# Kernel optimization log

Measured on AMD Instinct MI355X. Metric: run time of the kernel, lower is better.

## Reference

```python
import jax, jax.numpy as jnp
import numpy as np

ALPHA = 0.25   # FOCAL_LOSS_ALPHA
GAMMA = 2.0    # FOCAL_LOSS_GAMMA


def pairwise_iou(anchor, boxes):
    # anchor [A,4], boxes [M,4] -> [A,M]
    area_b = (boxes[:, 2] - boxes[:, 0]) * (boxes[:, 3] - boxes[:, 1])        # [M]
    area_a = (anchor[:, 2] - anchor[:, 0]) * (anchor[:, 3] - anchor[:, 1])    # [A]
    iw = jnp.clip(jnp.minimum(anchor[:, None, 2], boxes[None, :, 2]) -
                  jnp.maximum(anchor[:, None, 0], boxes[None, :, 0]), 0.0)
    ih = jnp.clip(jnp.minimum(anchor[:, None, 3], boxes[None, :, 3]) -
                  jnp.maximum(anchor[:, None, 1], boxes[None, :, 1]), 0.0)
    inter = iw * ih
    ua = jnp.clip(area_a[:, None] + area_b[None, :] - inter, 1e-8)
    return inter / ua


def _per_image(cls_pred, reg_pred, ann, anchor, aw, ah, acx, acy):
    # cls_pred [A,C], reg_pred [A,4], ann [M,5]
    valid = ann[:, 4] != -1.0                              # padding mask
    p = jnp.clip(cls_pred, 1e-4, 1.0 - 1e-4)
    iou = pairwise_iou(anchor, ann[:, :4])                 # [A,M]
    iou = jnp.where(valid[None, :], iou, -1.0)             # invalid GT never matched
    iou_max = iou.max(axis=1)
    iou_arg = iou.argmax(axis=1)
    assigned = ann[iou_arg]                                # [A,5]
    pos = iou_max >= 0.5
    num_pos = pos.sum().astype(p.dtype)
    C = p.shape[1]
    one_hot = jax.nn.one_hot(assigned[:, 4].astype(jnp.int32), C, dtype=p.dtype)
    # targets: 1 for assigned class on positives, 0 elsewhere on positives,
    # 0 everywhere for IoU<0.4, -1 (ignore) in between
    targets = jnp.where(pos[:, None], one_hot,
                        jnp.where((iou_max < 0.4)[:, None], 0.0, -1.0))
    af = jnp.where(targets == 1.0, ALPHA, 1.0 - ALPHA)
    fw = jnp.where(targets == 1.0, 1.0 - p, p)
    fw = af * fw ** GAMMA
    bce = -(targets * jnp.log(p) + (1.0 - targets) * jnp.log(1.0 - p))
    cls_loss = jnp.where(targets != -1.0, fw * bce, 0.0).sum() / jnp.maximum(num_pos, 1.0)
    gw = assigned[:, 2] - assigned[:, 0]
    gh = assigned[:, 3] - assigned[:, 1]
    gcx = assigned[:, 0] + 0.5 * gw
    gcy = assigned[:, 1] + 0.5 * gh
    gw = jnp.maximum(gw, 1.0)
    gh = jnp.maximum(gh, 1.0)
    t = jnp.stack([(gcx - acx) / aw, (gcy - acy) / ah,
                   jnp.log(gw / aw), jnp.log(gh / ah)], axis=1)
    t = t / jnp.array([[0.1, 0.1, 0.2, 0.2]], dtype=p.dtype)
    diff = jnp.abs(t - reg_pred)
    rl = jnp.where(diff <= 1.0 / 9.0, 0.5 * 9.0 * diff ** 2, diff - 0.5 / 9.0)
    reg_loss = jnp.where(num_pos > 0,
                         (rl * pos[:, None]).sum() / jnp.maximum(4.0 * num_pos, 1.0),
                         0.0)
    return cls_loss, reg_loss


def setup_inputs() -> dict:
    key = jax.random.key(0)
    kc, kr, ka1, ka2, kb1, kb2, kl = jax.random.split(key, 7)
    B, A, C, M = 8, 120000, 80, 32
    classifications = jax.random.uniform(kc, (B, A, C), jnp.float32, 0.001, 0.999)
    regressions = jax.random.normal(kr, (B, A, 4), jnp.float32)
    # anchors: valid boxes with x1<x2, y1<y2
    xy1 = jax.random.uniform(ka1, (1, A, 2), jnp.float32, 0.0, 700.0)
    wh = jax.random.uniform(ka2, (1, A, 2), jnp.float32, 8.0, 200.0)
    anchors = jnp.concatenate([xy1, xy1 + wh], axis=-1)
    # annotations: [B,M,5], last 8 slots per image padded with -1
    gxy1 = jax.random.uniform(kb1, (B, M, 2), jnp.float32, 0.0, 600.0)
    gwh = jax.random.uniform(kb2, (B, M, 2), jnp.float32, 16.0, 250.0)
    labels = jax.random.randint(kl, (B, M, 1), 0, C).astype(jnp.float32)
    annotations = jnp.concatenate([gxy1, gxy1 + gwh, labels], axis=-1)
    pad = jnp.arange(M) >= (M - 8)
    annotations = jnp.where(pad[None, :, None], -1.0, annotations)
    return {"classifications": classifications, "regressions": regressions,
            "anchors": anchors, "annotations": annotations}


def reference(classifications, regressions, anchors, annotations):
    anchor = anchors[0]
    aw = anchor[:, 2] - anchor[:, 0]
    ah = anchor[:, 3] - anchor[:, 1]
    acx = anchor[:, 0] + 0.5 * aw
    acy = anchor[:, 1] + 0.5 * ah
    cls_l, reg_l = jax.vmap(_per_image, in_axes=(0, 0, 0, None, None, None, None, None))(
        classifications, regressions, annotations, anchor, aw, ah, acx, acy)
    return cls_l.mean(keepdims=True), reg_l.mean(keepdims=True)
```

## Files before the change

### kernel.cpp

```cpp
#include <hip/hip_runtime.h>
#include <hip/hip_bf16.h>

constexpr int B_   = 8;
constexpr int A_   = 120000;
constexpr int C_   = 80;
constexpr int M_   = 32;
constexpr int APB  = 256;
constexpr int C4   = C_ / 4;
constexpr int GX   = (A_ + APB - 1) / APB;

#define F_LN2 0.69314718056f
#define C0_ (0.75f * F_LN2)
#define C1_ (0.25f * F_LN2)

typedef float vfloat4 __attribute__((ext_vector_type(4)));


__device__ __forceinline__ float smooth_l1(float d) {
    return (d <= (1.0f / 9.0f)) ? 4.5f * d * d : d - (0.5f / 9.0f);
}

__device__ __forceinline__ float clampp(float x) {
    return fminf(fmaxf(x, 1e-4f), 1.0f - 1e-4f);
}

__device__ __forceinline__ float f_neg(float p) {
    return C0_ * p * p * (-__log2f(1.0f - p));
}
__device__ __forceinline__ float f_pos(float p) {
    const float q = 1.0f - p;
    return C1_ * q * q * (-__log2f(p));
}

__global__ __launch_bounds__(256) void focal_fused(
    const float* __restrict__ cls,
    const float* __restrict__ reg,
    const float* __restrict__ anc,
    const float* __restrict__ ann,
    float* __restrict__ P_cls,
    float* __restrict__ P_reg,
    float* __restrict__ P_np)
{
    __shared__ float s_ann[M_ * 5];
    __shared__ float s_mask[APB];
    __shared__ float s_red[3][4];

    const int b   = blockIdx.y;
    const int a0  = blockIdx.x * APB;
    const int tid = threadIdx.x;
    const int na  = min(APB, A_ - a0);

    if (tid < M_ * 5) s_ann[tid] = ann[b * M_ * 5 + tid];
    __syncthreads();

    float acc  = 0.0f;
    float rsum = 0.0f;
    float npos = 0.0f;

    if (tid < na) {
        const int a = a0 + tid;
        const float4 ab = reinterpret_cast<const float4*>(anc)[a];
        const float ax1 = ab.x, ay1 = ab.y, ax2 = ab.z, ay2 = ab.w;
        const float area_a = (ax2 - ax1) * (ay2 - ay1);

        float best = -2.0f;
        int   arg  = 0;
        #pragma unroll 8
        for (int m = 0; m < M_; ++m) {
            const float bx1 = s_ann[m * 5 + 0];
            const float by1 = s_ann[m * 5 + 1];
            const float bx2 = s_ann[m * 5 + 2];
            const float by2 = s_ann[m * 5 + 3];
            const float lab = s_ann[m * 5 + 4];
            float iw = fmaxf(fminf(ax2, bx2) - fmaxf(ax1, bx1), 0.0f);
            float ih = fmaxf(fminf(ay2, by2) - fmaxf(ay1, by1), 0.0f);
            const float inter  = iw * ih;
            const float area_b = (bx2 - bx1) * (by2 - by1);
            const float ua = fmaxf(area_a + area_b - inter, 1e-8f);
            float iou = inter / ua;
            if (lab == -1.0f) iou = -1.0f;
            if (iou > best) { best = iou; arg = m; }
        }

        float mask = 1.0f;
        if (best >= 0.5f) {
            const int code = (int)s_ann[arg * 5 + 4];
            const float gx1 = s_ann[arg * 5 + 0];
            const float gy1 = s_ann[arg * 5 + 1];
            const float gx2 = s_ann[arg * 5 + 2];
            const float gy2 = s_ann[arg * 5 + 3];
            float gw = gx2 - gx1, gh = gy2 - gy1;
            const float gcx = gx1 + 0.5f * gw;
            const float gcy = gy1 + 0.5f * gh;
            gw = fmaxf(gw, 1.0f);
            gh = fmaxf(gh, 1.0f);
            const float aw  = ax2 - ax1, ah = ay2 - ay1;
            const float acx = ax1 + 0.5f * aw;
            const float acy = ay1 + 0.5f * ah;
            const float t0 = ((gcx - acx) / aw) * 10.0f;
            const float t1 = ((gcy - acy) / ah) * 10.0f;
            const float t2 = logf(gw / aw) * 5.0f;
            const float t3 = logf(gh / ah) * 5.0f;
            const float4 rp = reinterpret_cast<const float4*>(reg)[(size_t)b * A_ + a];
            rsum = smooth_l1(fabsf(t0 - rp.x))
                 + smooth_l1(fabsf(t1 - rp.y))
                 + smooth_l1(fabsf(t2 - rp.z))
                 + smooth_l1(fabsf(t3 - rp.w));
            npos = 1.0f;
            const float p = clampp(cls[((size_t)b * A_ + a) * C_ + code]);
            acc = f_pos(p) - f_neg(p);
        } else if (best >= 0.4f) {
            mask = 0.0f;
        }
        s_mask[tid] = mask;
    }
    __syncthreads();

    const vfloat4* cp = reinterpret_cast<const vfloat4*>(cls) + ((size_t)b * A_ + a0) * C4;
    const int total = na * C4;
    #pragma unroll 4
    for (int t = tid; t < total; t += APB) {
        const int la = t / C4;
        const float m = s_mask[la];
        const vfloat4 v = __builtin_nontemporal_load(&cp[t]);
        float s = f_neg(clampp(v.x));
        s += f_neg(clampp(v.y));
        s += f_neg(clampp(v.z));
        s += f_neg(clampp(v.w));
        acc = fmaf(m, s, acc);
    }

    #pragma unroll
    for (int off = 32; off > 0; off >>= 1) {
        acc  += __shfl_down(acc,  off, 64);
        rsum += __shfl_down(rsum, off, 64);
        npos += __shfl_down(npos, off, 64);
    }
    const int wv = tid >> 6;
    if ((tid & 63) == 0) {
        s_red[0][wv] = acc;
        s_red[1][wv] = rsum;
        s_red[2][wv] = npos;
    }
    __syncthreads();
    if (tid == 0) {
        const int slot = b * GX + blockIdx.x;
        P_cls[slot] = s_red[0][0] + s_red[0][1] + s_red[0][2] + s_red[0][3];
        P_reg[slot] = s_red[1][0] + s_red[1][1] + s_red[1][2] + s_red[1][3];
        P_np [slot] = s_red[2][0] + s_red[2][1] + s_red[2][2] + s_red[2][3];
    }
}

__global__ __launch_bounds__(1024) void focal_finalize(
    const float* __restrict__ P_cls,
    const float* __restrict__ P_reg,
    const float* __restrict__ P_np,
    float* __restrict__ out)
{
    __shared__ float red[3][16];
    const int tid  = threadIdx.x;
    const int lane = tid & 63;
    const int wv   = tid >> 6;
    float cm = 0.0f, rm = 0.0f;

    for (int b = 0; b < B_; ++b) {
        float c = 0.0f, r = 0.0f, n = 0.0f;
        for (int x = tid; x < GX; x += 1024) {
            c += P_cls[b * GX + x];
            r += P_reg[b * GX + x];
            n += P_np [b * GX + x];
        }
        #pragma unroll
        for (int off = 32; off > 0; off >>= 1) {
            c += __shfl_down(c, off, 64);
            r += __shfl_down(r, off, 64);
            n += __shfl_down(n, off, 64);
        }
        if (lane == 0) { red[0][wv] = c; red[1][wv] = r; red[2][wv] = n; }
        __syncthreads();
        if (tid == 0) {
            float cs = 0.0f, rs = 0.0f, ns = 0.0f;
            #pragma unroll
            for (int w = 0; w < 16; ++w) { cs += red[0][w]; rs += red[1][w]; ns += red[2][w]; }
            cm += cs / fmaxf(ns, 1.0f);
            rm += (ns > 0.0f) ? rs / fmaxf(4.0f * ns, 1.0f) : 0.0f;
        }
        __syncthreads();
    }
    if (tid == 0) {
        out[0] = cm / (float)B_;
        out[1] = rm / (float)B_;
    }
}

extern "C" void kernel_launch(void* const* d_in, const int* in_sizes, int n_in,
                              void* d_out, int out_size, void* d_ws, size_t ws_size,
                              hipStream_t stream) {
    const float* cls = (const float*)d_in[0];
    const float* reg = (const float*)d_in[1];
    const float* anc = (const float*)d_in[2];
    const float* ann = (const float*)d_in[3];
    float* out = (float*)d_out;

    float* wsf   = (float*)d_ws;
    float* P_cls = wsf;
    float* P_reg = wsf + B_ * GX;
    float* P_np  = wsf + 2 * B_ * GX;

    dim3 grid(GX, B_);
    focal_fused<<<grid, APB, 0, stream>>>(cls, reg, anc, ann, P_cls, P_reg, P_np);
    focal_finalize<<<1, 1024, 0, stream>>>(P_cls, P_reg, P_np, out);
}
```

Measured before the change: 407.4 us.

## Split fused kernel into assignment pass and pure streaming classification pass

The single fused kernel is split in two. The first kernel computes the IoU assignment per anchor and writes a per-anchor mask to workspace, together with the regression, positive-count and correction partial sums. The second kernel streams the classification tensor and applies the mask it reads from global memory. The intent is for the bandwidth-bound stream to run without the compute-heavy IoU phase and block barrier in front of it. It also uses a hardware reciprocal and log2 for cheaper math, drops the nontemporal loads, and parallelizes the finalize kernel across images. The cost is an extra launch and an extra round trip of the mask through global memory.

```diff
diff --git a/kernel.cpp b/kernel.cpp
--- a/kernel.cpp
+++ b/kernel.cpp
@@ -13,8 +13,11 @@
 #define C0_ (0.75f * F_LN2)
 #define C1_ (0.25f * F_LN2)
 
-typedef float vfloat4 __attribute__((ext_vector_type(4)));
-
+constexpr size_t WS_MASK   = 0;
+constexpr size_t WS_PA_REG = (size_t)B_ * A_;
+constexpr size_t WS_PA_NP  = WS_PA_REG + (size_t)B_ * GX;
+constexpr size_t WS_PA_COR = WS_PA_NP  + (size_t)B_ * GX;
+constexpr size_t WS_PB_CLS = WS_PA_COR + (size_t)B_ * GX;
 
 __device__ __forceinline__ float smooth_l1(float d) {
     return (d <= (1.0f / 9.0f)) ? 4.5f * d * d : d - (0.5f / 9.0f);
@@ -32,17 +35,17 @@
     return C1_ * q * q * (-__log2f(p));
 }
 
-__global__ __launch_bounds__(256) void focal_fused(
+__global__ __launch_bounds__(256) void assign_k(
     const float* __restrict__ cls,
     const float* __restrict__ reg,
     const float* __restrict__ anc,
     const float* __restrict__ ann,
-    float* __restrict__ P_cls,
-    float* __restrict__ P_reg,
-    float* __restrict__ P_np)
+    float* __restrict__ mask,
+    float* __restrict__ PA_reg,
+    float* __restrict__ PA_np,
+    float* __restrict__ PA_cor)
 {
     __shared__ float s_ann[M_ * 5];
-    __shared__ float s_mask[APB];
     __shared__ float s_red[3][4];
 
     const int b   = blockIdx.y;
@@ -53,9 +56,7 @@
     if (tid < M_ * 5) s_ann[tid] = ann[b * M_ * 5 + tid];
     __syncthreads();
 
-    float acc  = 0.0f;
-    float rsum = 0.0f;
-    float npos = 0.0f;
+    float rsum = 0.0f, npos = 0.0f, corr = 0.0f;
 
     if (tid < na) {
         const int a = a0 + tid;
@@ -65,24 +66,24 @@
 
         float best = -2.0f;
         int   arg  = 0;
-        #pragma unroll 8
+        #pragma unroll
         for (int m = 0; m < M_; ++m) {
             const float bx1 = s_ann[m * 5 + 0];
             const float by1 = s_ann[m * 5 + 1];
             const float bx2 = s_ann[m * 5 + 2];
             const float by2 = s_ann[m * 5 + 3];
             const float lab = s_ann[m * 5 + 4];
-            float iw = fmaxf(fminf(ax2, bx2) - fmaxf(ax1, bx1), 0.0f);
-            float ih = fmaxf(fminf(ay2, by2) - fmaxf(ay1, by1), 0.0f);
+            const float iw = fmaxf(fminf(ax2, bx2) - fmaxf(ax1, bx1), 0.0f);
+            const float ih = fmaxf(fminf(ay2, by2) - fmaxf(ay1, by1), 0.0f);
             const float inter  = iw * ih;
             const float area_b = (bx2 - bx1) * (by2 - by1);
             const float ua = fmaxf(area_a + area_b - inter, 1e-8f);
-            float iou = inter / ua;
+            float iou = inter * __builtin_amdgcn_rcpf(ua);
             if (lab == -1.0f) iou = -1.0f;
             if (iou > best) { best = iou; arg = m; }
         }
 
-        float mask = 1.0f;
+        float mk = 1.0f;
         if (best >= 0.5f) {
             const int code = (int)s_ann[arg * 5 + 4];
             const float gx1 = s_ann[arg * 5 + 0];
@@ -99,8 +100,8 @@
             const float acy = ay1 + 0.5f * ah;
             const float t0 = ((gcx - acx) / aw) * 10.0f;
             const float t1 = ((gcy - acy) / ah) * 10.0f;
-            const float t2 = logf(gw / aw) * 5.0f;
-            const float t3 = logf(gh / ah) * 5.0f;
+            const float t2 = __log2f(gw / aw) * (5.0f * F_LN2);
+            const float t3 = __log2f(gh / ah) * (5.0f * F_LN2);
             const float4 rp = reinterpret_cast<const float4*>(reg)[(size_t)b * A_ + a];
             rsum = smooth_l1(fabsf(t0 - rp.x))
                  + smooth_l1(fabsf(t1 - rp.y))
@@ -108,86 +109,99 @@
                  + smooth_l1(fabsf(t3 - rp.w));
             npos = 1.0f;
             const float p = clampp(cls[((size_t)b * A_ + a) * C_ + code]);
-            acc = f_pos(p) - f_neg(p);
+            corr = f_pos(p) - f_neg(p);
         } else if (best >= 0.4f) {
-            mask = 0.0f;
+            mk = 0.0f;
         }
-        s_mask[tid] = mask;
-    }
-    __syncthreads();
-
-    const vfloat4* cp = reinterpret_cast<const vfloat4*>(cls) + ((size_t)b * A_ + a0) * C4;
+        mask[(size_t)b * A_ + a] = mk;
+    }
+
+    #pragma unroll
+    for (int off = 32; off > 0; off >>= 1) {
+        rsum += __shfl_down(rsum, off, 64);
+        npos += __shfl_down(npos, off, 64);
+        corr += __shfl_down(corr, off, 64);
+    }
+    const int wv = tid >> 6;
+    if ((tid & 63) == 0) { s_red[0][wv] = rsum; s_red[1][wv] = npos; s_red[2][wv] = corr; }
+    __syncthreads();
+    if (tid == 0) {
+        const int slot = b * GX + blockIdx.x;
+        PA_reg[slot] = s_red[0][0] + s_red[0][1] + s_red[0][2] + s_red[0][3];
+        PA_np [slot] = s_red[1][0] + s_red[1][1] + s_red[1][2] + s_red[1][3];
+        PA_cor[slot] = s_red[2][0] + s_red[2][1] + s_red[2][2] + s_red[2][3];
+    }
+}
+
+__global__ __launch_bounds__(256) void stream_k(
+    const float* __restrict__ cls,
+    const float* __restrict__ mask,
+    float* __restrict__ PB_cls)
+{
+    __shared__ float s_red[4];
+
+    const int b   = blockIdx.y;
+    const int a0  = blockIdx.x * APB;
+    const int tid = threadIdx.x;
+    const int na  = min(APB, A_ - a0);
     const int total = na * C4;
+
+    const float4* cp = reinterpret_cast<const float4*>(cls) + ((size_t)b * A_ + a0) * C4;
+    const float*  mb = mask + (size_t)b * A_ + a0;
+
+    float acc = 0.0f;
     #pragma unroll 4
     for (int t = tid; t < total; t += APB) {
         const int la = t / C4;
-        const float m = s_mask[la];
-        const vfloat4 v = __builtin_nontemporal_load(&cp[t]);
+        const float4 v = cp[t];
         float s = f_neg(clampp(v.x));
         s += f_neg(clampp(v.y));
         s += f_neg(clampp(v.z));
         s += f_neg(clampp(v.w));
-        acc = fmaf(m, s, acc);
-    }
-
+        acc = fmaf(mb[la], s, acc);
+    }
+
+    #pragma unroll
+    for (int off = 32; off > 0; off >>= 1) acc += __shfl_down(acc, off, 64);
+    if ((tid & 63) == 0) s_red[tid >> 6] = acc;
+    __syncthreads();
+    if (tid == 0)
+        PB_cls[b * GX + blockIdx.x] = s_red[0] + s_red[1] + s_red[2] + s_red[3];
+}
+
+__global__ __launch_bounds__(512) void fin_k(
+    const float* __restrict__ PA_reg,
+    const float* __restrict__ PA_np,
+    const float* __restrict__ PA_cor,
+    const float* __restrict__ PB_cls,
+    float* __restrict__ out)
+{
+    __shared__ float s_cm[8], s_rm[8];
+    const int tid  = threadIdx.x;
+    const int lane = tid & 63;
+    const int b    = tid >> 6;
+
+    float c = 0.0f, r = 0.0f, n = 0.0f;
+    for (int x = lane; x < GX; x += 64) {
+        c += PB_cls[b * GX + x] + PA_cor[b * GX + x];
+        r += PA_reg[b * GX + x];
+        n += PA_np [b * GX + x];
+    }
     #pragma unroll
     for (int off = 32; off > 0; off >>= 1) {
-        acc  += __shfl_down(acc,  off, 64);
-        rsum += __shfl_down(rsum, off, 64);
-        npos += __shfl_down(npos, off, 64);
-    }
-    const int wv = tid >> 6;
-    if ((tid & 63) == 0) {
-        s_red[0][wv] = acc;
-        s_red[1][wv] = rsum;
-        s_red[2][wv] = npos;
+        c += __shfl_down(c, off, 64);
+        r += __shfl_down(r, off, 64);
+        n += __shfl_down(n, off, 64);
+    }
+    if (lane == 0) {
+        s_cm[b] = c / fmaxf(n, 1.0f);
+        s_rm[b] = (n > 0.0f) ? r / fmaxf(4.0f * n, 1.0f) : 0.0f;
     }
     __syncthreads();
     if (tid == 0) {
-        const int slot = b * GX + blockIdx.x;
-        P_cls[slot] = s_red[0][0] + s_red[0][1] + s_red[0][2] + s_red[0][3];
-        P_reg[slot] = s_red[1][0] + s_red[1][1] + s_red[1][2] + s_red[1][3];
-        P_np [slot] = s_red[2][0] + s_red[2][1] + s_red[2][2] + s_red[2][3];
-    }
-}
-
-__global__ __launch_bounds__(1024) void focal_finalize(
-    const float* __restrict__ P_cls,
-    const float* __restrict__ P_reg,
-    const float* __restrict__ P_np,
-    float* __restrict__ out)
-{
-    __shared__ float red[3][16];
-    const int tid  = threadIdx.x;
-    const int lane = tid & 63;
-    const int wv   = tid >> 6;
-    float cm = 0.0f, rm = 0.0f;
-
-    for (int b = 0; b < B_; ++b) {
-        float c = 0.0f, r = 0.0f, n = 0.0f;
-        for (int x = tid; x < GX; x += 1024) {
-            c += P_cls[b * GX + x];
-            r += P_reg[b * GX + x];
-            n += P_np [b * GX + x];
-        }
+        float cm = 0.0f, rm = 0.0f;
         #pragma unroll
-        for (int off = 32; off > 0; off >>= 1) {
-            c += __shfl_down(c, off, 64);
-            r += __shfl_down(r, off, 64);
-            n += __shfl_down(n, off, 64);
-        }
-        if (lane == 0) { red[0][wv] = c; red[1][wv] = r; red[2][wv] = n; }
-        __syncthreads();
-        if (tid == 0) {
-            float cs = 0.0f, rs = 0.0f, ns = 0.0f;
-            #pragma unroll
-            for (int w = 0; w < 16; ++w) { cs += red[0][w]; rs += red[1][w]; ns += red[2][w]; }
-            cm += cs / fmaxf(ns, 1.0f);
-            rm += (ns > 0.0f) ? rs / fmaxf(4.0f * ns, 1.0f) : 0.0f;
-        }
-        __syncthreads();
-    }
-    if (tid == 0) {
+        for (int i = 0; i < B_; ++i) { cm += s_cm[i]; rm += s_rm[i]; }
         out[0] = cm / (float)B_;
         out[1] = rm / (float)B_;
     }
@@ -202,12 +216,15 @@
     const float* ann = (const float*)d_in[3];
     float* out = (float*)d_out;
 
-    float* wsf   = (float*)d_ws;
-    float* P_cls = wsf;
-    float* P_reg = wsf + B_ * GX;
-    float* P_np  = wsf + 2 * B_ * GX;
+    float* wsf    = (float*)d_ws;
+    float* mask   = wsf + WS_MASK;
+    float* PA_reg = wsf + WS_PA_REG;
+    float* PA_np  = wsf + WS_PA_NP;
+    float* PA_cor = wsf + WS_PA_COR;
+    float* PB_cls = wsf + WS_PB_CLS;
 
     dim3 grid(GX, B_);
-    focal_fused<<<grid, APB, 0, stream>>>(cls, reg, anc, ann, P_cls, P_reg, P_np);
-    focal_finalize<<<1, 1024, 0, stream>>>(P_cls, P_reg, P_np, out);
-}
+    assign_k<<<grid, APB, 0, stream>>>(cls, reg, anc, ann, mask, PA_reg, PA_np, PA_cor);
+    stream_k<<<grid, APB, 0, stream>>>(cls, mask, PB_cls);
+    fin_k<<<1, 512, 0, stream>>>(PA_reg, PA_np, PA_cor, PB_cls, out);
+}
```

Result: slower. 443.9 us (+8.9%).
